# Optimization experiments

Hardware: AMD Instinct MI355X
Metric: run time of the kernel (lower is better)

## Reference

```python
import jax, jax.numpy as jnp
from jax import lax
import numpy as np

SCALE = 1.0   # self.scale
EPS = 1e-12
CHUNK = 512   # points processed per chunk to bound [P,T,3] temporaries


def _closest_sqdist(p, a, b, c):
    """Squared distance from points p:[P,3] to triangles (a,b,c):[T,3] -> [P,T].
    Ericson's closest-point-on-triangle, fully vectorized."""
    ab = b - a
    ac = c - a
    bc = c - b
    ap = p[:, None, :] - a[None, :, :]
    bp = p[:, None, :] - b[None, :, :]
    cp = p[:, None, :] - c[None, :, :]
    d1 = jnp.einsum('td,ptd->pt', ab, ap)
    d2 = jnp.einsum('td,ptd->pt', ac, ap)
    d3 = jnp.einsum('td,ptd->pt', ab, bp)
    d4 = jnp.einsum('td,ptd->pt', ac, bp)
    d5 = jnp.einsum('td,ptd->pt', ab, cp)
    d6 = jnp.einsum('td,ptd->pt', ac, cp)
    va = d3 * d6 - d5 * d4
    vb = d5 * d2 - d1 * d6
    vc = d1 * d4 - d3 * d2

    def sdiv(n, d):  # NaN/Inf-safe division (branch is masked out by where anyway)
        return n / jnp.where(jnp.abs(d) < EPS, 1.0, d)

    t_ab = sdiv(d1, d1 - d3)[..., None]
    t_ac = sdiv(d2, d2 - d6)[..., None]
    t_bc = sdiv(d4 - d3, (d4 - d3) + (d5 - d6))[..., None]
    denom = va + vb + vc
    v_in = sdiv(vb, denom)[..., None]
    w_in = sdiv(vc, denom)[..., None]

    # base case: interior of the face; then overwrite with edge / vertex regions
    cl = a[None] + v_in * ab[None] + w_in * ac[None]
    cl = jnp.where(((va <= 0) & (d4 - d3 >= 0) & (d5 - d6 >= 0))[..., None],
                   b[None] + t_bc * bc[None], cl)   # edge BC
    cl = jnp.where(((vb <= 0) & (d2 >= 0) & (d6 <= 0))[..., None],
                   a[None] + t_ac * ac[None], cl)   # edge AC
    cl = jnp.where(((vc <= 0) & (d1 >= 0) & (d3 <= 0))[..., None],
                   a[None] + t_ab * ab[None], cl)   # edge AB
    cl = jnp.where(((d6 >= 0) & (d5 <= d6))[..., None], c[None], cl)  # vertex C
    cl = jnp.where(((d3 >= 0) & (d4 <= d3))[..., None], b[None], cl)  # vertex B
    cl = jnp.where(((d1 <= 0) & (d2 <= 0))[..., None], a[None], cl)   # vertex A
    diff = p[:, None, :] - cl
    return jnp.sum(diff * diff, axis=-1)


def setup_inputs():
    key = jax.random.key(0)
    k1, k2, k3 = jax.random.split(key, 3)
    vertices = jax.random.normal(k1, (4, 3, 16, 16, 16), dtype=jnp.float32)
    pc = jax.random.uniform(k2, (4, 4096, 3), dtype=jnp.float32)
    faces = jax.random.randint(k3, (8192, 3), 0, 4096, dtype=jnp.int32)
    return {"vertices": vertices, "pc": pc, "faces": faces}


def reference(vertices, pc, faces):
    B = vertices.shape[0]
    v = jax.nn.sigmoid(vertices)                     # self.normalization
    pos = jnp.moveaxis(v, 1, -1).reshape(B, -1, 3)   # permute(1,2,3,0).view(-1,3)
    pts = pc * SCALE                                 # _scale_points
    # pymesh path drops all-zero points; emulate with a mask (scaling keeps zeros zero)
    mask = jnp.any(pc != 0.0, axis=-1).astype(pts.dtype)  # [B,N]

    def per_batch(args):
        posb, pb, mb = args
        a = posb[faces[:, 0]]
        b = posb[faces[:, 1]]
        c = posb[faces[:, 2]]
        n_chunks = pb.shape[0] // CHUNK

        def chunk_min(pch):  # [CHUNK,3] -> [CHUNK] nearest sq-dist over all tris
            return jnp.min(_closest_sqdist(pch, a, b, c), axis=-1)

        d = lax.map(chunk_min, pb.reshape(n_chunks, CHUNK, 3)).reshape(-1)
        cnt = jnp.maximum(jnp.sum(mb), 1.0)
        return jnp.sum(d * mb) / cnt                 # mean(squared_distances)

    losses = lax.map(per_batch, (pos, pts, mask))    # [B]
    return jnp.mean(losses)
```

## Files before the change

### kernel.cpp

```cpp
#include <hip/hip_runtime.h>
#include <math.h>
#include <float.h>

#define NB 4
#define NP 4096
#define NT 8192
#define TSE 12
#define TEE 20
#define EPSD 1e-12
#define MNS 32
#define MTCH (NT/MNS)
#define NSEED 2048
#define VCH 8
#define VLEN (NSEED/VCH)
#define DENSE_T 32

#define PREP_BLKS (NB*NT/256)
#define PSORT_BASE PREP_BLKS
#define SEED_BASE  (PSORT_BASE + NB)
#define SEED_BLKS  (NB*VCH*16)
#define INIT_BASE  (SEED_BASE + SEED_BLKS)
#define INIT_BLKS  (NB*NP/256)
#define FUSED_BLKS (INIT_BASE + INIT_BLKS)

__device__ __forceinline__ float sigm(float x) { return 1.0f / (1.0f + expf(-x)); }

__device__ __forceinline__ float tri_dist(
    float px, float py, float pz,
    float ax, float ay, float az,
    float abx, float aby, float abz,
    float acx, float acy, float acz,
    float aa, float am, float cc,
    float raa, float rcc, float rbb,
    float rden, float den, float bb, float k1)
{
  float apx = px - ax, apy = py - ay, apz = pz - az;
  float d1   = apx*abx + apy*aby + apz*abz;
  float d2   = apx*acx + apy*acy + apz*acz;
  float apap = apx*apx + apy*apy + apz*apz;
  float vb = d1*cc - d2*am;
  float vc = d2*aa - d1*am;
  float va = den - vb - vc;
  float di = apap - (vb*d1 + vc*d2)*rden;
  float t2 = d1 + d1;
  float tab = fminf(fmaxf(d1*raa, 0.0f), 1.0f);
  float dAB = apap + tab*(tab*aa - t2);
  float t4 = d2 + d2;
  float tac = fminf(fmaxf(d2*rcc, 0.0f), 1.0f);
  float dAC = apap + tac*(tac*cc - t4);
  float e   = d2 - d1 + k1;
  float tbc = fminf(fmaxf(e*rbb, 0.0f), 1.0f);
  float distB = apap - t2 + aa;
  float dBC = distB + tbc*(tbc*bb - (e + e));
  float m3 = fminf(fminf(dAB, dAC), dBC);
  bool in = (vb >= 0.0f) & (vc >= 0.0f) & (va > 0.0f);
  return in ? di : m3;
}

__global__ __launch_bounds__(256) void fused_prep_kernel(
    const float* __restrict__ verts, const int* __restrict__ faces,
    const float* __restrict__ pc,
    float* __restrict__ triS, float* __restrict__ triE,
    unsigned* __restrict__ perm, float* __restrict__ partS,
    unsigned* __restrict__ partF, unsigned* __restrict__ cnt)
{
  int blk = blockIdx.x;
  int tid = threadIdx.x;

  if (blk < PREP_BLKS) {
    if (blk == 0 && tid == 0) *cnt = 0u;
    int idx = blk * 256 + tid;
    int b = idx >> 13;
    int t = idx & (NT - 1);
    int f0 = faces[3*t + 0], f1 = faces[3*t + 1], f2i = faces[3*t + 2];
    const float* vb_ = verts + (size_t)b * 3 * NP;
    float ax = sigm(vb_[f0]),  ay = sigm(vb_[NP + f0]),  az = sigm(vb_[2*NP + f0]);
    float bx = sigm(vb_[f1]),  by = sigm(vb_[NP + f1]),  bz = sigm(vb_[2*NP + f1]);
    float cx = sigm(vb_[f2i]), cy = sigm(vb_[NP + f2i]), cz = sigm(vb_[2*NP + f2i]);
    float abx = bx - ax, aby = by - ay, abz = bz - az;
    float acx = cx - ax, acy = cy - ay, acz = cz - az;
    double aa = (double)abx*abx + (double)aby*aby + (double)abz*abz;
    double am = (double)abx*acx + (double)aby*acy + (double)abz*acz;
    double cc = (double)acx*acx + (double)acy*acy + (double)acz*acz;
    double den = aa*cc - am*am;
    double bb  = aa - 2.0*am + cc;
    float raa  = (fabs(aa)  < EPSD) ? 1.0f : (float)(1.0/aa);
    float rcc  = (fabs(cc)  < EPSD) ? 1.0f : (float)(1.0/cc);
    float rbb  = (fabs(bb)  < EPSD) ? 1.0f : (float)(1.0/bb);
    float rden = (fabs(den) < EPSD) ? 0.0f : (float)(1.0/den);
    double nx = (double)aby*acz - (double)abz*acy;
    double ny = (double)abz*acx - (double)abx*acz;
    double nz = (double)abx*acy - (double)aby*acx;
    double rs = (fabs(den) < EPSD) ? 0.0 : 1.0 / sqrt(den * 1.02);
    float nhx = (float)(nx * rs), nhy = (float)(ny * rs), nhz = (float)(nz * rs);
    float w = (float)(-(nx*ax + ny*ay + nz*az) * rs);
    float lox = fminf(ax, fminf(bx, cx)), hix = fmaxf(ax, fmaxf(bx, cx));
    float loy = fminf(ay, fminf(by, cy)), hiy = fmaxf(ay, fmaxf(by, cy));
    float loz = fminf(az, fminf(bz, cz)), hiz = fmaxf(az, fmaxf(bz, cz));
    float* rs_ = triS + (size_t)idx * TSE;
    rs_[0] = nhx; rs_[1] = nhy; rs_[2]  = nhz;  rs_[3]  = w;
    rs_[4] = lox; rs_[5] = loy; rs_[6]  = loz;  rs_[7]  = hix;
    rs_[8] = hiy; rs_[9] = hiz; rs_[10] = 0.0f; rs_[11] = 0.0f;
    float* re = triE + (size_t)idx * TEE;
    re[0]  = ax;  re[1]  = ay;  re[2]  = az;  re[3]  = abx;
    re[4]  = aby; re[5]  = abz; re[6]  = acx; re[7]  = acy;
    re[8]  = acz; re[9]  = (float)aa; re[10] = (float)am; re[11] = (float)cc;
    re[12] = raa; re[13] = rcc; re[14] = rbb; re[15] = rden;
    re[16] = (float)den; re[17] = (float)bb; re[18] = (float)(aa - am); re[19] = 0.0f;

  } else if (blk < SEED_BASE) {
    __shared__ unsigned hist[64];
    __shared__ unsigned off[64];
    int b = blk - PSORT_BASE;
    if (tid < 64) hist[tid] = 0u;
    __syncthreads();
    unsigned cells[16], ranks[16];
    #pragma unroll
    for (int k = 0; k < 16; ++k) {
      int i = k * 256 + tid;
      const float* pp = pc + ((size_t)b * NP + i) * 3;
      float x = pp[0], y = pp[1], z = pp[2];
      int ix = min(3, max(0, (int)(x * 4.0f)));
      int iy = min(3, max(0, (int)(y * 4.0f)));
      int iz = min(3, max(0, (int)(z * 4.0f)));
      unsigned c = (unsigned)(ix | (iy << 2) | (iz << 4));
      cells[k] = c;
      ranks[k] = atomicAdd(&hist[c], 1u);
    }
    __syncthreads();
    if (tid == 0) {
      unsigned acc = 0u;
      for (int c = 0; c < 64; ++c) { off[c] = acc; acc += hist[c]; }
    }
    __syncthreads();
    #pragma unroll
    for (int k = 0; k < 16; ++k) {
      int i = k * 256 + tid;
      perm[(size_t)b * NP + off[cells[k]] + ranks[k]] = (unsigned)i;
    }

  } else if (blk < INIT_BASE) {
    __shared__ float sx[VLEN], sy[VLEN], sz[VLEN];
    int sid  = blk - SEED_BASE;
    int pblk = sid & 15;
    int vc   = (sid >> 4) & (VCH - 1);
    int b    = sid >> 7;
    int t    = vc * VLEN + tid;
    int f0   = faces[3 * t];
    const float* vb_ = verts + (size_t)b * 3 * NP;
    sx[tid] = sigm(vb_[f0]);
    sy[tid] = sigm(vb_[NP + f0]);
    sz[tid] = sigm(vb_[2 * NP + f0]);
    __syncthreads();
    int p = pblk * 256 + tid;
    const float* pp = pc + ((size_t)b * NP + p) * 3;
    float px = pp[0], py = pp[1], pz = pp[2];
    float m = FLT_MAX;
    #pragma unroll 4
    for (int j = 0; j < VLEN; ++j) {
      float dx = px - sx[j], dy = py - sy[j], dz = pz - sz[j];
      m = fminf(m, dx*dx + dy*dy + dz*dz);
    }
    partS[((size_t)b * VCH + vc) * NP + p] = m;

  } else {
    int i = (blk - INIT_BASE) * 256 + tid;
    partF[i] = 0x7F7FFFFFu;
  }
}

__global__ __launch_bounds__(256) void main_kernel(
    const float* __restrict__ triS, const float* __restrict__ triE,
    const float* __restrict__ pc, const float* __restrict__ partS,
    const unsigned* __restrict__ perm, unsigned* __restrict__ partF)
{
  __shared__ unsigned qbuf[4][128];
  __shared__ unsigned wmind[4][64];

  int bid  = blockIdx.x;
  int pblk = bid & 15;
  int s    = (bid >> 4) & (MNS - 1);
  int b    = bid >> 9;
  int tid  = threadIdx.x;
  int wave = tid >> 6, lane = tid & 63;
  int p    = (int)perm[(size_t)b * NP + pblk * 256 + tid];

  const float* pp = pc + ((size_t)b * NP + p) * 3;
  float px = pp[0], py = pp[1], pz = pp[2];

  float mind = FLT_MAX;
  #pragma unroll
  for (int j = 0; j < VCH; ++j)
    mind = fminf(mind, partS[((size_t)b * VCH + j) * NP + p]);
  wmind[wave][lane] = __float_as_uint(mind);
  float mth = mind + 1e-8f;

  unsigned qcnt = 0u, qd = 0u;
  const float* triEB = triE + (size_t)b * NT * TEE;
  int tg0 = s * MTCH;
  const float4* Rs = (const float4*)(triS + (size_t)(b * NT + tg0) * TSE);

#define DRAIN_BATCH(NACT)                                                     \
  {                                                                           \
    unsigned ent = qbuf[wave][(qd + (unsigned)lane) & 127u];                  \
    if ((unsigned)lane < (unsigned)(NACT)) {                                  \
      int te  = (int)(ent >> 6);                                              \
      int src = (int)(ent & 63u);                                             \
      float qx = __shfl(px, src, 64);                                         \
      float qy = __shfl(py, src, 64);                                         \
      float qz = __shfl(pz, src, 64);                                         \
      const float* rr = triEB + (size_t)te * TEE;                             \
      float4 w1 = *(const float4*)(rr + 0);                                   \
      float4 w2 = *(const float4*)(rr + 4);                                   \
      float4 w3 = *(const float4*)(rr + 8);                                   \
      float4 w4 = *(const float4*)(rr + 12);                                  \
      float4 w5 = *(const float4*)(rr + 16);                                  \
      float dd = fmaxf(tri_dist(qx, qy, qz,                                   \
                                w1.x, w1.y, w1.z,                             \
                                w1.w, w2.x, w2.y,                             \
                                w2.z, w2.w, w3.x,                             \
                                w3.y, w3.z, w3.w,                             \
                                w4.x, w4.y, w4.z,                             \
                                w4.w, w5.x, w5.y, w5.z), 0.0f);               \
      atomicMin(&wmind[wave][src], __float_as_uint(dd));                      \
    }                                                                         \
    qd += (unsigned)(NACT);                                                   \
    mind = fminf(mind, __uint_as_float(wmind[wave][lane]));                   \
    mth  = mind + 1e-8f;                                                      \
  }

#define SCAN_ITER(Q0, Q1, Q2, TIDX)                                           \
  {                                                                           \
    float sN = fmaf(pz, (Q0).z, fmaf(py, (Q0).y, fmaf(px, (Q0).x, (Q0).w)));  \
    float dx = fmaxf(fmaxf((Q1).x - px, px - (Q1).w), 0.0f);                  \
    float dy = fmaxf(fmaxf((Q1).y - py, py - (Q2).x), 0.0f);                  \
    float dz = fmaxf(fmaxf((Q1).z - pz, pz - (Q2).y), 0.0f);                  \
    float bb2 = fmaf(dx, dx, fmaf(dy, dy, dz * dz));                          \
    bool pred = (sN * sN < mth) & (bb2 * 0.98f < mth);                        \
    unsigned long long mask = __ballot(pred);                                 \
    if (mask) {                                                               \
      int nsv = __builtin_popcountll(mask);                                   \
      if (nsv >= DENSE_T) {                                                   \
        const float* rr = triEB + (size_t)(TIDX) * TEE;                       \
        float4 w1 = *(const float4*)(rr + 0);                                 \
        float4 w2 = *(const float4*)(rr + 4);                                 \
        float4 w3 = *(const float4*)(rr + 8);                                 \
        float4 w4 = *(const float4*)(rr + 12);                                \
        float4 w5 = *(const float4*)(rr + 16);                                \
        float dd = fmaxf(tri_dist(px, py, pz,                                 \
                                  w1.x, w1.y, w1.z,                           \
                                  w1.w, w2.x, w2.y,                           \
                                  w2.z, w2.w, w3.x,                           \
                                  w3.y, w3.z, w3.w,                           \
                                  w4.x, w4.y, w4.z,                           \
                                  w4.w, w5.x, w5.y, w5.z), 0.0f);             \
        mind = fminf(mind, dd);                                               \
        mth  = mind + 1e-8f;                                                  \
      } else {                                                                \
        if (pred) {                                                           \
          int prefix = __builtin_amdgcn_mbcnt_hi((unsigned)(mask >> 32),      \
                         __builtin_amdgcn_mbcnt_lo((unsigned)mask, 0));       \
          qbuf[wave][(qcnt + (unsigned)prefix) & 127u] =                      \
              ((unsigned)(TIDX) << 6) | (unsigned)lane;                       \
        }                                                                     \
        qcnt += (unsigned)nsv;                                                \
        if (qcnt - qd >= 64u) DRAIN_BATCH(64u);                               \
      }                                                                       \
    }                                                                         \
  }

  float4 a0 = Rs[0], a1 = Rs[1], a2 = Rs[2];
  float4 b0 = Rs[3], b1 = Rs[4], b2 = Rs[5];
  int tg = tg0;
  for (int g = 0; g < MTCH / 2; ++g) {
    const float4* Rn = Rs + 6;
    float4 c0 = Rn[0], c1 = Rn[1], c2 = Rn[2];
    float4 d0 = Rn[3], d1 = Rn[4], d2 = Rn[5];
    SCAN_ITER(a0, a1, a2, tg + 0);
    SCAN_ITER(b0, b1, b2, tg + 1);
    a0 = c0; a1 = c1; a2 = c2;
    b0 = d0; b1 = d1; b2 = d2;
    Rs = Rn; tg += 2;
  }

  unsigned pend = qcnt - qd;
  if (pend) DRAIN_BATCH(pend);
  mind = fminf(mind, __uint_as_float(wmind[wave][lane]));

  atomicMin(&partF[(size_t)b * NP + p], __float_as_uint(fmaxf(mind, 0.0f)));

#undef SCAN_ITER
#undef DRAIN_BATCH
}

__global__ __launch_bounds__(256) void reduce_kernel(
    const float* __restrict__ partF, const float* __restrict__ pc,
    float* __restrict__ bl2, unsigned* __restrict__ cnt,
    float* __restrict__ out)
{
  int blk = blockIdx.x;
  int b = blk >> 4;
  int p = (blk & 15) * 256 + threadIdx.x;
  float m = partF[(size_t)b * NP + p];
  const float* pp = pc + ((size_t)b * NP + p) * 3;
  float x = pp[0], y = pp[1], z = pp[2];
  float msk = ((x != 0.0f) | (y != 0.0f) | (z != 0.0f)) ? 1.0f : 0.0f;
  float sdm = m * msk, sm = msk;
  for (int off = 32; off > 0; off >>= 1) {
    sdm += __shfl_down(sdm, off, 64);
    sm  += __shfl_down(sm,  off, 64);
  }
  __shared__ float s1[4], s2[4];
  __shared__ bool last;
  int wave = threadIdx.x >> 6, lanei = threadIdx.x & 63;
  if (lanei == 0) { s1[wave] = sdm; s2[wave] = sm; }
  __syncthreads();
  if (threadIdx.x == 0) {
    bl2[2 * blk]     = s1[0] + s1[1] + s1[2] + s1[3];
    bl2[2 * blk + 1] = s2[0] + s2[1] + s2[2] + s2[3];
    __threadfence();
    unsigned t = atomicAdd(cnt, 1u);
    last = (t == 63u);
  }
  __syncthreads();
  if (last) {
    __shared__ float f1[64], f2[64];
    if (threadIdx.x < 64) {
      f1[threadIdx.x] = atomicAdd(&bl2[2 * threadIdx.x],     0.0f);
      f2[threadIdx.x] = atomicAdd(&bl2[2 * threadIdx.x + 1], 0.0f);
    }
    __syncthreads();
    if (threadIdx.x == 0) {
      float acc = 0.0f;
      for (int bb = 0; bb < NB; ++bb) {
        float tsd = 0.0f, tsm = 0.0f;
        for (int k = 0; k < 16; ++k) {
          tsd += f1[bb * 16 + k];
          tsm += f2[bb * 16 + k];
        }
        acc += tsd / fmaxf(tsm, 1.0f);
      }
      out[0] = 0.25f * acc;
    }
  }
}

extern "C" void kernel_launch(void* const* d_in, const int* in_sizes, int n_in,
                              void* d_out, int out_size, void* d_ws, size_t ws_size,
                              hipStream_t stream) {
  const float* verts = (const float*)d_in[0];
  const float* pc    = (const float*)d_in[1];
  const int*   faces = (const int*)d_in[2];
  float* out = (float*)d_out;

  float* triS  = (float*)d_ws;
  float* triE  = triS  + (size_t)NB * NT * TSE;
  float* partS = triE  + (size_t)NB * NT * TEE;
  float* partF = partS + (size_t)NB * VCH * NP;
  float* bl2   = partF + (size_t)NB * NP;
  unsigned* cnt  = (unsigned*)(bl2 + 128);
  unsigned* perm = (unsigned*)(bl2 + 132);

  fused_prep_kernel<<<FUSED_BLKS, 256, 0, stream>>>(
      verts, faces, pc, triS, triE, perm, partS, (unsigned*)partF, cnt);
  main_kernel<<<NB * MNS * 16, 256, 0, stream>>>(
      triS, triE, pc, partS, perm, (unsigned*)partF);
  reduce_kernel<<<NB * 16, 256, 0, stream>>>(partF, pc, bl2, cnt, out);
}
```

Measured before the change: 190.4 us.

## Fuse reduction into main kernel, drop dense path, disable culling for thin triangles

The final reduction kernel is removed. The last main_kernel block, detected with a global atomic counter, now sums partF over all points and writes the mean. The dense-evaluation fast path inside the scan is dropped, so every candidate triangle goes through the queued batch drain. Near-degenerate triangles now get a zero plane and infinite bounds in prep, so the cull always accepts them. These changes save one launch and simplify the scan branch, at the cost of a serial tail reduction done by a single block and possibly more queued work.

```diff
diff --git a/kernel.cpp b/kernel.cpp
--- a/kernel.cpp
+++ b/kernel.cpp
@@ -13,7 +13,6 @@
 #define NSEED 2048
 #define VCH 8
 #define VLEN (NSEED/VCH)
-#define DENSE_T 32
 
 #define PREP_BLKS (NB*NT/256)
 #define PSORT_BASE PREP_BLKS
@@ -22,6 +21,8 @@
 #define INIT_BASE  (SEED_BASE + SEED_BLKS)
 #define INIT_BLKS  (NB*NP/256)
 #define FUSED_BLKS (INIT_BASE + INIT_BLKS)
+
+#define MAIN_BLKS (NB*MNS*16)
 
 __device__ __forceinline__ float sigm(float x) { return 1.0f / (1.0f + expf(-x)); }
 
@@ -97,6 +98,11 @@
     float lox = fminf(ax, fminf(bx, cx)), hix = fmaxf(ax, fmaxf(bx, cx));
     float loy = fminf(ay, fminf(by, cy)), hiy = fmaxf(ay, fmaxf(by, cy));
     float loz = fminf(az, fminf(bz, cz)), hiz = fmaxf(az, fmaxf(bz, cz));
+    if (den < 0.05 * aa * cc) {
+      nhx = 0.0f; nhy = 0.0f; nhz = 0.0f; w = 0.0f;
+      lox = -1e30f; loy = -1e30f; loz = -1e30f;
+      hix =  1e30f; hiy =  1e30f; hiz =  1e30f;
+    }
     float* rs_ = triS + (size_t)idx * TSE;
     rs_[0] = nhx; rs_[1] = nhy; rs_[2]  = nhz;  rs_[3]  = w;
     rs_[4] = lox; rs_[5] = loy; rs_[6]  = loz;  rs_[7]  = hix;
@@ -172,10 +178,13 @@
 __global__ __launch_bounds__(256) void main_kernel(
     const float* __restrict__ triS, const float* __restrict__ triE,
     const float* __restrict__ pc, const float* __restrict__ partS,
-    const unsigned* __restrict__ perm, unsigned* __restrict__ partF)
+    const unsigned* __restrict__ perm, unsigned* __restrict__ partF,
+    unsigned* __restrict__ cnt, float* __restrict__ out)
 {
   __shared__ unsigned qbuf[4][128];
   __shared__ unsigned wmind[4][64];
+  __shared__ float s1[4], s2[4];
+  __shared__ bool last;
 
   int bid  = blockIdx.x;
   int pblk = bid & 15;
@@ -239,33 +248,14 @@
     bool pred = (sN * sN < mth) & (bb2 * 0.98f < mth);                        \
     unsigned long long mask = __ballot(pred);                                 \
     if (mask) {                                                               \
-      int nsv = __builtin_popcountll(mask);                                   \
-      if (nsv >= DENSE_T) {                                                   \
-        const float* rr = triEB + (size_t)(TIDX) * TEE;                       \
-        float4 w1 = *(const float4*)(rr + 0);                                 \
-        float4 w2 = *(const float4*)(rr + 4);                                 \
-        float4 w3 = *(const float4*)(rr + 8);                                 \
-        float4 w4 = *(const float4*)(rr + 12);                                \
-        float4 w5 = *(const float4*)(rr + 16);                                \
-        float dd = fmaxf(tri_dist(px, py, pz,                                 \
-                                  w1.x, w1.y, w1.z,                           \
-                                  w1.w, w2.x, w2.y,                           \
-                                  w2.z, w2.w, w3.x,                           \
-                                  w3.y, w3.z, w3.w,                           \
-                                  w4.x, w4.y, w4.z,                           \
-                                  w4.w, w5.x, w5.y, w5.z), 0.0f);             \
-        mind = fminf(mind, dd);                                               \
-        mth  = mind + 1e-8f;                                                  \
-      } else {                                                                \
-        if (pred) {                                                           \
-          int prefix = __builtin_amdgcn_mbcnt_hi((unsigned)(mask >> 32),      \
-                         __builtin_amdgcn_mbcnt_lo((unsigned)mask, 0));       \
-          qbuf[wave][(qcnt + (unsigned)prefix) & 127u] =                      \
-              ((unsigned)(TIDX) << 6) | (unsigned)lane;                       \
-        }                                                                     \
-        qcnt += (unsigned)nsv;                                                \
-        if (qcnt - qd >= 64u) DRAIN_BATCH(64u);                               \
+      if (pred) {                                                             \
+        int prefix = __builtin_amdgcn_mbcnt_hi((unsigned)(mask >> 32),        \
+                       __builtin_amdgcn_mbcnt_lo((unsigned)mask, 0));         \
+        qbuf[wave][(qcnt + (unsigned)prefix) & 127u] =                        \
+            ((unsigned)(TIDX) << 6) | (unsigned)lane;                         \
       }                                                                       \
+      qcnt += (unsigned)__builtin_popcountll(mask);                           \
+      if (qcnt - qd >= 64u) DRAIN_BATCH(64u);                                 \
     }                                                                         \
   }
 
@@ -291,58 +281,42 @@
 
 #undef SCAN_ITER
 #undef DRAIN_BATCH
-}
-
-__global__ __launch_bounds__(256) void reduce_kernel(
-    const float* __restrict__ partF, const float* __restrict__ pc,
-    float* __restrict__ bl2, unsigned* __restrict__ cnt,
-    float* __restrict__ out)
-{
-  int blk = blockIdx.x;
-  int b = blk >> 4;
-  int p = (blk & 15) * 256 + threadIdx.x;
-  float m = partF[(size_t)b * NP + p];
-  const float* pp = pc + ((size_t)b * NP + p) * 3;
-  float x = pp[0], y = pp[1], z = pp[2];
-  float msk = ((x != 0.0f) | (y != 0.0f) | (z != 0.0f)) ? 1.0f : 0.0f;
-  float sdm = m * msk, sm = msk;
-  for (int off = 32; off > 0; off >>= 1) {
-    sdm += __shfl_down(sdm, off, 64);
-    sm  += __shfl_down(sm,  off, 64);
-  }
-  __shared__ float s1[4], s2[4];
-  __shared__ bool last;
-  int wave = threadIdx.x >> 6, lanei = threadIdx.x & 63;
-  if (lanei == 0) { s1[wave] = sdm; s2[wave] = sm; }
+
   __syncthreads();
-  if (threadIdx.x == 0) {
-    bl2[2 * blk]     = s1[0] + s1[1] + s1[2] + s1[3];
-    bl2[2 * blk + 1] = s2[0] + s2[1] + s2[2] + s2[3];
+  if (tid == 0) {
     __threadfence();
     unsigned t = atomicAdd(cnt, 1u);
-    last = (t == 63u);
+    last = (t == (unsigned)(MAIN_BLKS - 1));
   }
   __syncthreads();
-  if (last) {
-    __shared__ float f1[64], f2[64];
-    if (threadIdx.x < 64) {
-      f1[threadIdx.x] = atomicAdd(&bl2[2 * threadIdx.x],     0.0f);
-      f2[threadIdx.x] = atomicAdd(&bl2[2 * threadIdx.x + 1], 0.0f);
-    }
-    __syncthreads();
-    if (threadIdx.x == 0) {
-      float acc = 0.0f;
-      for (int bb = 0; bb < NB; ++bb) {
-        float tsd = 0.0f, tsm = 0.0f;
-        for (int k = 0; k < 16; ++k) {
-          tsd += f1[bb * 16 + k];
-          tsm += f2[bb * 16 + k];
-        }
-        acc += tsd / fmaxf(tsm, 1.0f);
+  if (!last) return;
+
+  float acc = 0.0f;
+  for (int bb_ = 0; bb_ < NB; ++bb_) {
+    float tsd = 0.0f, tsm = 0.0f;
+    for (int k = 0; k < 16; ++k) {
+      int pi = k * 256 + tid;
+      unsigned mu = atomicAdd(&partF[(size_t)bb_ * NP + pi], 0u);
+      float m = __uint_as_float(mu);
+      const float* q = pc + ((size_t)bb_ * NP + pi) * 3;
+      float x = q[0], y = q[1], z = q[2];
+      float msk = ((x != 0.0f) | (y != 0.0f) | (z != 0.0f)) ? 1.0f : 0.0f;
+      float sdm = m * msk, sm = msk;
+      for (int off = 32; off > 0; off >>= 1) {
+        sdm += __shfl_down(sdm, off, 64);
+        sm  += __shfl_down(sm,  off, 64);
       }
-      out[0] = 0.25f * acc;
-    }
-  }
+      if (lane == 0) { s1[wave] = sdm; s2[wave] = sm; }
+      __syncthreads();
+      if (tid == 0) {
+        tsd += s1[0] + s1[1] + s1[2] + s1[3];
+        tsm += s2[0] + s2[1] + s2[2] + s2[3];
+      }
+      __syncthreads();
+    }
+    if (tid == 0) acc += tsd / fmaxf(tsm, 1.0f);
+  }
+  if (tid == 0) out[0] = 0.25f * acc;
 }
 
 extern "C" void kernel_launch(void* const* d_in, const int* in_sizes, int n_in,
@@ -357,13 +331,11 @@
   float* triE  = triS  + (size_t)NB * NT * TSE;
   float* partS = triE  + (size_t)NB * NT * TEE;
   float* partF = partS + (size_t)NB * VCH * NP;
-  float* bl2   = partF + (size_t)NB * NP;
-  unsigned* cnt  = (unsigned*)(bl2 + 128);
-  unsigned* perm = (unsigned*)(bl2 + 132);
+  unsigned* cnt  = (unsigned*)(partF + (size_t)NB * NP);
+  unsigned* perm = (unsigned*)(cnt + 4);
 
   fused_prep_kernel<<<FUSED_BLKS, 256, 0, stream>>>(
       verts, faces, pc, triS, triE, perm, partS, (unsigned*)partF, cnt);
-  main_kernel<<<NB * MNS * 16, 256, 0, stream>>>(
-      triS, triE, pc, partS, perm, (unsigned*)partF);
-  reduce_kernel<<<NB * 16, 256, 0, stream>>>(partF, pc, bl2, cnt, out);
+  main_kernel<<<MAIN_BLKS, 256, 0, stream>>>(
+      triS, triE, pc, partS, perm, (unsigned*)partF, cnt, out);
 }
```

After: 246.3 us. 29.3% more time.
